# Performance work log

Hardware: AMD Instinct MI355X
Metric: run time of the kernel (lower is better)

The kernel has to match this reference:

```python
import jax, jax.numpy as jnp
import numpy as np

B, M, I = 32, 8192, 256
TEMPERATURE = 1.0


def setup_inputs() -> dict:
    key = jax.random.key(0)
    k1, k2, k3, k4 = jax.random.split(key, 4)
    memory = jax.random.normal(k1, (B, M, I), dtype=jnp.float32)
    qkey = jax.random.normal(k2, (B, I), dtype=jnp.float32)
    beta = jax.random.uniform(k3, (B,), dtype=jnp.float32)
    # xavier-uniform init for Linear(I, I)
    limit = float(np.sqrt(6.0 / (I + I)))
    W = jax.random.uniform(k4, (I, I), dtype=jnp.float32, minval=-limit, maxval=limit)
    b = jnp.zeros((I,), dtype=jnp.float32)
    return {"memory": memory, "key": qkey, "beta": beta, "W": W, "b": b}


def reference(memory, key, beta, W, b):
    # projected_key = tanh(key @ W^T + b)  -- torch Linear stores weight [out, in]
    projected_key = jnp.tanh(key @ W.T + b)                      # [B, I]
    diff = projected_key[:, None, :] - memory                    # [B, M, I]
    distances = jnp.sum(diff * diff, axis=-1)                    # [B, M]
    similarity = -distances
    weights = jax.nn.softmax(beta[:, None] * similarity / TEMPERATURE, axis=-1)  # [B, M]
    read_vector = jnp.einsum('bm,bmi->bi', weights, memory)      # [B, I]
    return weights, read_vector, similarity
```

## Files before the change

### kernel.cpp

```cpp
#include <hip/hip_runtime.h>
#include <math.h>

constexpr int Bdim = 32;
constexpr int Mdim = 8192;
constexpr int Idim = 256;
constexpr int ROWS_PER_BLOCK = 128;
constexpr int ROWS_PER_WAVE = 32;
constexpr int NCHUNK = Mdim / ROWS_PER_BLOCK;

__global__ void proj_key_kernel(const float* __restrict__ key,
                                const float* __restrict__ W,
                                const float* __restrict__ bias,
                                float* __restrict__ pk) {
    int b = blockIdx.x;
    int i = threadIdx.x;
    __shared__ float kq[Idim];
    kq[i] = key[b * Idim + i];
    __syncthreads();
    const float4* w4 = (const float4*)(W + (size_t)i * Idim);
    const float4* k4 = (const float4*)kq;
    float s = bias[i];
    #pragma unroll 4
    for (int k = 0; k < Idim / 4; ++k) {
        float4 wv = w4[k];
        float4 kv = k4[k];
        s += wv.x * kv.x + wv.y * kv.y + wv.z * kv.z + wv.w * kv.w;
    }
    pk[b * Idim + i] = tanhf(s);
}

__global__ void fused_pass1_kernel(const float* __restrict__ memory,
                                   const float* __restrict__ pk,
                                   const float* __restrict__ beta,
                                   float* __restrict__ sim,
                                   float* __restrict__ pvec,
                                   float* __restrict__ pmx,
                                   float* __restrict__ psum) {
    int b = blockIdx.x / NCHUNK;
    int c = blockIdx.x % NCHUNK;
    int wave = threadIdx.x >> 6;
    int lane = threadIdx.x & 63;
    float bt = beta[b];

    float4 pkv = ((const float4*)(pk + b * Idim))[lane];

    int row0 = c * ROWS_PER_BLOCK + wave * ROWS_PER_WAVE;
    const float* base = memory + ((size_t)b * Mdim + row0) * Idim;
    float* simp = sim + (size_t)b * Mdim + row0;

    float mx = -INFINITY, ssum = 0.f;
    float4 acc = make_float4(0.f, 0.f, 0.f, 0.f);
    float my_sim = 0.f;

    for (int r = 0; r < ROWS_PER_WAVE; ++r) {
        float4 mv = ((const float4*)(base + (size_t)r * Idim))[lane];
        float dx = pkv.x - mv.x, dy = pkv.y - mv.y;
        float dz = pkv.z - mv.z, dw = pkv.w - mv.w;
        float s = dx * dx + dy * dy + dz * dz + dw * dw;
        #pragma unroll
        for (int off = 32; off; off >>= 1) s += __shfl_xor(s, off, 64);
        if (lane == r) my_sim = -s;

        float a = -bt * s;
        float nmx = fmaxf(mx, a);
        float scale = __expf(mx - nmx);
        float p = __expf(a - nmx);
        ssum = ssum * scale + p;
        acc.x = acc.x * scale + p * mv.x;
        acc.y = acc.y * scale + p * mv.y;
        acc.z = acc.z * scale + p * mv.z;
        acc.w = acc.w * scale + p * mv.w;
        mx = nmx;
    }
    if (lane < ROWS_PER_WAVE) simp[lane] = my_sim;

    __shared__ float lacc[4][Idim];
    __shared__ float lmx[4], lsum[4];
    ((float4*)lacc[wave])[lane] = acc;
    if (lane == 0) { lmx[wave] = mx; lsum[wave] = ssum; }
    __syncthreads();

    float MX = fmaxf(fmaxf(lmx[0], lmx[1]), fmaxf(lmx[2], lmx[3]));
    float e0 = __expf(lmx[0] - MX), e1 = __expf(lmx[1] - MX);
    float e2 = __expf(lmx[2] - MX), e3 = __expf(lmx[3] - MX);
    int i = threadIdx.x;
    float v = lacc[0][i] * e0 + lacc[1][i] * e1 + lacc[2][i] * e2 + lacc[3][i] * e3;
    size_t pc = (size_t)b * NCHUNK + c;
    pvec[pc * Idim + i] = v;
    if (threadIdx.x == 0) {
        pmx[pc] = MX;
        psum[pc] = lsum[0] * e0 + lsum[1] * e1 + lsum[2] * e2 + lsum[3] * e3;
    }
}

__global__ void combine_kernel(const float* __restrict__ pvec,
                               const float* __restrict__ pmx,
                               const float* __restrict__ psum,
                               float* __restrict__ read_vec,
                               float* __restrict__ MXb,
                               float* __restrict__ invb) {
    int b = blockIdx.x;
    int tid = threadIdx.x;
    __shared__ float e[NCHUNK];
    __shared__ float sInv;

    if (tid < NCHUNK) {
        float m = pmx[(size_t)b * NCHUNK + tid];
        float mm = m;
        #pragma unroll
        for (int off = 32; off; off >>= 1) mm = fmaxf(mm, __shfl_xor(mm, off, 64));
        float ec = __expf(m - mm);
        e[tid] = ec;
        float sc = psum[(size_t)b * NCHUNK + tid] * ec;
        #pragma unroll
        for (int off = 32; off; off >>= 1) sc += __shfl_xor(sc, off, 64);
        if (tid == 0) {
            sInv = 1.f / sc;
            MXb[b] = mm;
            invb[b] = 1.f / sc;
        }
    }
    __syncthreads();

    float v = 0.f;
    const float* p = pvec + (size_t)b * NCHUNK * Idim + tid;
    #pragma unroll 8
    for (int c = 0; c < NCHUNK; ++c) v += p[(size_t)c * Idim] * e[c];
    read_vec[(size_t)b * Idim + tid] = v * sInv;
}

__global__ void weights_kernel(const float* __restrict__ sim,
                               const float* __restrict__ beta,
                               const float* __restrict__ MXb,
                               const float* __restrict__ invb,
                               float* __restrict__ weights) {
    int g = (blockIdx.x * 256 + threadIdx.x) * 4;
    int b = g >> 13;
    float bt = beta[b], MX = MXb[b], inv = invb[b];
    float4 s = *(const float4*)(sim + g);
    float4 w;
    w.x = __expf(bt * s.x - MX) * inv;
    w.y = __expf(bt * s.y - MX) * inv;
    w.z = __expf(bt * s.z - MX) * inv;
    w.w = __expf(bt * s.w - MX) * inv;
    *(float4*)(weights + g) = w;
}

extern "C" void kernel_launch(void* const* d_in, const int* in_sizes, int n_in,
                              void* d_out, int out_size, void* d_ws, size_t ws_size,
                              hipStream_t stream) {
    const float* memory = (const float*)d_in[0];
    const float* key    = (const float*)d_in[1];
    const float* beta   = (const float*)d_in[2];
    const float* W      = (const float*)d_in[3];
    const float* bias   = (const float*)d_in[4];

    float* out = (float*)d_out;
    float* weights  = out;
    float* read_vec = out + (size_t)Bdim * Mdim;
    float* sim      = read_vec + (size_t)Bdim * Idim;

    float* pk   = (float*)d_ws;
    float* pvec = pk + (size_t)Bdim * Idim;
    float* pmx  = pvec + (size_t)Bdim * NCHUNK * Idim;
    float* psum = pmx + (size_t)Bdim * NCHUNK;
    float* MXb  = psum + (size_t)Bdim * NCHUNK;
    float* invb = MXb + Bdim;

    proj_key_kernel<<<Bdim, Idim, 0, stream>>>(key, W, bias, pk);
    fused_pass1_kernel<<<Bdim * NCHUNK, 256, 0, stream>>>(memory, pk, beta,
                                                          sim, pvec, pmx, psum);
    combine_kernel<<<Bdim, Idim, 0, stream>>>(pvec, pmx, psum, read_vec, MXb, invb);
    weights_kernel<<<(Bdim * Mdim) / 1024, 256, 0, stream>>>(sim, beta, MXb, invb, weights);
}
```

Before: 63.94 us.

## Process two rows per wave iteration, lazy rescale, fuse combine with weights kernel

The main pass now splits each wave into two half-waves that each handle one memory row per iteration. Each lane loads two float4s, and the cross-lane reduction drops to 5 shuffles plus one exchange. The online softmax rescales only when a new maximum appears, which removes one exp per row in the common case, and the block reduction now merges 8 partial states. The separate weights kernel is folded into the combine kernel. That saves one launch and the MX/inv round trip, but only 32 blocks are left to write the weights.

```diff
diff --git a/kernel.cpp b/kernel.cpp
--- a/kernel.cpp
+++ b/kernel.cpp
@@ -40,69 +40,104 @@
     int c = blockIdx.x % NCHUNK;
     int wave = threadIdx.x >> 6;
     int lane = threadIdx.x & 63;
+    int half = lane >> 5;
+    int sub  = lane & 31;
     float bt = beta[b];
 
-    float4 pkv = ((const float4*)(pk + b * Idim))[lane];
+    const float4* pk4 = (const float4*)(pk + b * Idim);
+    float4 pk0 = pk4[sub * 2];
+    float4 pk1 = pk4[sub * 2 + 1];
 
     int row0 = c * ROWS_PER_BLOCK + wave * ROWS_PER_WAVE;
     const float* base = memory + ((size_t)b * Mdim + row0) * Idim;
     float* simp = sim + (size_t)b * Mdim + row0;
 
     float mx = -INFINITY, ssum = 0.f;
-    float4 acc = make_float4(0.f, 0.f, 0.f, 0.f);
+    float4 acc0 = make_float4(0.f, 0.f, 0.f, 0.f);
+    float4 acc1 = make_float4(0.f, 0.f, 0.f, 0.f);
     float my_sim = 0.f;
 
-    for (int r = 0; r < ROWS_PER_WAVE; ++r) {
-        float4 mv = ((const float4*)(base + (size_t)r * Idim))[lane];
-        float dx = pkv.x - mv.x, dy = pkv.y - mv.y;
-        float dz = pkv.z - mv.z, dw = pkv.w - mv.w;
-        float s = dx * dx + dy * dy + dz * dz + dw * dw;
-        #pragma unroll
-        for (int off = 32; off; off >>= 1) s += __shfl_xor(s, off, 64);
-        if (lane == r) my_sim = -s;
+    for (int t = 0; t < ROWS_PER_WAVE / 2; ++t) {
+        const float* rp = base + (size_t)(2 * t + half) * Idim + sub * 8;
+        float4 m0 = *(const float4*)rp;
+        float4 m1 = *(const float4*)(rp + 4);
+
+        float d, s;
+        d = pk0.x - m0.x; s  = d * d;
+        d = pk0.y - m0.y; s += d * d;
+        d = pk0.z - m0.z; s += d * d;
+        d = pk0.w - m0.w; s += d * d;
+        d = pk1.x - m1.x; s += d * d;
+        d = pk1.y - m1.y; s += d * d;
+        d = pk1.z - m1.z; s += d * d;
+        d = pk1.w - m1.w; s += d * d;
+        #pragma unroll
+        for (int off = 16; off; off >>= 1) s += __shfl_xor(s, off, 64);
+        float s_other = __shfl_xor(s, 32, 64);
+        if ((lane >> 1) == t) my_sim = (lane & 1) ? -s_other : -s;
 
         float a = -bt * s;
-        float nmx = fmaxf(mx, a);
-        float scale = __expf(mx - nmx);
-        float p = __expf(a - nmx);
-        ssum = ssum * scale + p;
-        acc.x = acc.x * scale + p * mv.x;
-        acc.y = acc.y * scale + p * mv.y;
-        acc.z = acc.z * scale + p * mv.z;
-        acc.w = acc.w * scale + p * mv.w;
-        mx = nmx;
-    }
-    if (lane < ROWS_PER_WAVE) simp[lane] = my_sim;
-
-    __shared__ float lacc[4][Idim];
-    __shared__ float lmx[4], lsum[4];
-    ((float4*)lacc[wave])[lane] = acc;
-    if (lane == 0) { lmx[wave] = mx; lsum[wave] = ssum; }
+        if (a > mx) {
+            float scale = __expf(mx - a);
+            ssum *= scale;
+            acc0.x *= scale; acc0.y *= scale; acc0.z *= scale; acc0.w *= scale;
+            acc1.x *= scale; acc1.y *= scale; acc1.z *= scale; acc1.w *= scale;
+            mx = a;
+        }
+        float p = __expf(a - mx);
+        ssum += p;
+        acc0.x = fmaf(p, m0.x, acc0.x);
+        acc0.y = fmaf(p, m0.y, acc0.y);
+        acc0.z = fmaf(p, m0.z, acc0.z);
+        acc0.w = fmaf(p, m0.w, acc0.w);
+        acc1.x = fmaf(p, m1.x, acc1.x);
+        acc1.y = fmaf(p, m1.y, acc1.y);
+        acc1.z = fmaf(p, m1.z, acc1.z);
+        acc1.w = fmaf(p, m1.w, acc1.w);
+    }
+    if (lane < 32) simp[lane] = my_sim;
+
+    __shared__ float lacc[8][Idim];
+    __shared__ float lmx[8], lsum[8];
+    int wh = wave * 2 + half;
+    ((float4*)(lacc[wh] + sub * 8))[0] = acc0;
+    ((float4*)(lacc[wh] + sub * 8))[1] = acc1;
+    if (sub == 0) { lmx[wh] = mx; lsum[wh] = ssum; }
     __syncthreads();
 
-    float MX = fmaxf(fmaxf(lmx[0], lmx[1]), fmaxf(lmx[2], lmx[3]));
-    float e0 = __expf(lmx[0] - MX), e1 = __expf(lmx[1] - MX);
-    float e2 = __expf(lmx[2] - MX), e3 = __expf(lmx[3] - MX);
+    float MX = lmx[0];
+    #pragma unroll
+    for (int h = 1; h < 8; ++h) MX = fmaxf(MX, lmx[h]);
+    float e[8];
+    #pragma unroll
+    for (int h = 0; h < 8; ++h) e[h] = __expf(lmx[h] - MX);
+
     int i = threadIdx.x;
-    float v = lacc[0][i] * e0 + lacc[1][i] * e1 + lacc[2][i] * e2 + lacc[3][i] * e3;
+    float v = 0.f;
+    #pragma unroll
+    for (int h = 0; h < 8; ++h) v += lacc[h][i] * e[h];
     size_t pc = (size_t)b * NCHUNK + c;
     pvec[pc * Idim + i] = v;
     if (threadIdx.x == 0) {
+        float sc = 0.f;
+        #pragma unroll
+        for (int h = 0; h < 8; ++h) sc += lsum[h] * e[h];
         pmx[pc] = MX;
-        psum[pc] = lsum[0] * e0 + lsum[1] * e1 + lsum[2] * e2 + lsum[3] * e3;
-    }
-}
-
-__global__ void combine_kernel(const float* __restrict__ pvec,
-                               const float* __restrict__ pmx,
-                               const float* __restrict__ psum,
-                               float* __restrict__ read_vec,
-                               float* __restrict__ MXb,
-                               float* __restrict__ invb) {
+        psum[pc] = sc;
+    }
+}
+
+__global__ void combine_weights_kernel(const float* __restrict__ pvec,
+                                       const float* __restrict__ pmx,
+                                       const float* __restrict__ psum,
+                                       const float* __restrict__ sim,
+                                       const float* __restrict__ beta,
+                                       float* __restrict__ read_vec,
+                                       float* __restrict__ weights) {
     int b = blockIdx.x;
     int tid = threadIdx.x;
     __shared__ float e[NCHUNK];
-    __shared__ float sInv;
+    __shared__ float MXs, sInvs;
 
     if (tid < NCHUNK) {
         float m = pmx[(size_t)b * NCHUNK + tid];
@@ -114,36 +149,30 @@
         float sc = psum[(size_t)b * NCHUNK + tid] * ec;
         #pragma unroll
         for (int off = 32; off; off >>= 1) sc += __shfl_xor(sc, off, 64);
-        if (tid == 0) {
-            sInv = 1.f / sc;
-            MXb[b] = mm;
-            invb[b] = 1.f / sc;
-        }
+        if (tid == 0) { MXs = mm; sInvs = 1.f / sc; }
     }
     __syncthreads();
+
+    float MX = MXs, inv = sInvs;
 
     float v = 0.f;
     const float* p = pvec + (size_t)b * NCHUNK * Idim + tid;
     #pragma unroll 8
     for (int c = 0; c < NCHUNK; ++c) v += p[(size_t)c * Idim] * e[c];
-    read_vec[(size_t)b * Idim + tid] = v * sInv;
-}
-
-__global__ void weights_kernel(const float* __restrict__ sim,
-                               const float* __restrict__ beta,
-                               const float* __restrict__ MXb,
-                               const float* __restrict__ invb,
-                               float* __restrict__ weights) {
-    int g = (blockIdx.x * 256 + threadIdx.x) * 4;
-    int b = g >> 13;
-    float bt = beta[b], MX = MXb[b], inv = invb[b];
-    float4 s = *(const float4*)(sim + g);
-    float4 w;
-    w.x = __expf(bt * s.x - MX) * inv;
-    w.y = __expf(bt * s.y - MX) * inv;
-    w.z = __expf(bt * s.z - MX) * inv;
-    w.w = __expf(bt * s.w - MX) * inv;
-    *(float4*)(weights + g) = w;
+    read_vec[(size_t)b * Idim + tid] = v * inv;
+
+    float bt = beta[b];
+    const float4* s4 = (const float4*)(sim + (size_t)b * Mdim);
+    float4* w4 = (float4*)(weights + (size_t)b * Mdim);
+    for (int m4 = tid; m4 < Mdim / 4; m4 += 256) {
+        float4 s = s4[m4];
+        float4 w;
+        w.x = __expf(bt * s.x - MX) * inv;
+        w.y = __expf(bt * s.y - MX) * inv;
+        w.z = __expf(bt * s.z - MX) * inv;
+        w.w = __expf(bt * s.w - MX) * inv;
+        w4[m4] = w;
+    }
 }
 
 extern "C" void kernel_launch(void* const* d_in, const int* in_sizes, int n_in,
@@ -164,12 +193,10 @@
     float* pvec = pk + (size_t)Bdim * Idim;
     float* pmx  = pvec + (size_t)Bdim * NCHUNK * Idim;
     float* psum = pmx + (size_t)Bdim * NCHUNK;
-    float* MXb  = psum + (size_t)Bdim * NCHUNK;
-    float* invb = MXb + Bdim;
 
     proj_key_kernel<<<Bdim, Idim, 0, stream>>>(key, W, bias, pk);
     fused_pass1_kernel<<<Bdim * NCHUNK, 256, 0, stream>>>(memory, pk, beta,
                                                           sim, pvec, pmx, psum);
-    combine_kernel<<<Bdim, Idim, 0, stream>>>(pvec, pmx, psum, read_vec, MXb, invb);
-    weights_kernel<<<(Bdim * Mdim) / 1024, 256, 0, stream>>>(sim, beta, MXb, invb, weights);
-}
+    combine_weights_kernel<<<Bdim, 256, 0, stream>>>(pvec, pmx, psum, sim, beta,
+                                                     read_vec, weights);
+}
```

Result: slower. 65.37 us (+2.2%).

## Prefetch rows in pass1, lazy rescale, and fuse combine with weights kernel

Applied to the files above, without the earlier changes.

The main pass loop now software-prefetches memory rows two ahead. The online softmax rescales only when a new maximum appears, using FMAs, which saves an exp per row in the common case. The combine and weights kernels are merged into one epilogue launch of Bdim*NSLICE blocks. Each block recomputes the per-batch max and normalizer, and slice 0 also produces the read vector. This removes one kernel launch and the intermediate MXb/invb buffers, at the cost of redundant per-slice reductions and a divergent branch in the inner loop.

```diff
diff --git a/kernel.cpp b/kernel.cpp
--- a/kernel.cpp
+++ b/kernel.cpp
@@ -7,6 +7,7 @@
 constexpr int ROWS_PER_BLOCK = 128;
 constexpr int ROWS_PER_WAVE = 32;
 constexpr int NCHUNK = Mdim / ROWS_PER_BLOCK;
+constexpr int NSLICE = 8;
 
 __global__ void proj_key_kernel(const float* __restrict__ key,
                                 const float* __restrict__ W,
@@ -52,27 +53,42 @@
     float4 acc = make_float4(0.f, 0.f, 0.f, 0.f);
     float my_sim = 0.f;
 
-    for (int r = 0; r < ROWS_PER_WAVE; ++r) {
-        float4 mv = ((const float4*)(base + (size_t)r * Idim))[lane];
+    auto body = [&](float4 mv, int r) {
         float dx = pkv.x - mv.x, dy = pkv.y - mv.y;
         float dz = pkv.z - mv.z, dw = pkv.w - mv.w;
         float s = dx * dx + dy * dy + dz * dz + dw * dw;
         #pragma unroll
         for (int off = 32; off; off >>= 1) s += __shfl_xor(s, off, 64);
         if (lane == r) my_sim = -s;
+        float a = -bt * s;
+        if (a > mx) {
+            float sc = __expf(mx - a);
+            ssum *= sc;
+            acc.x *= sc; acc.y *= sc; acc.z *= sc; acc.w *= sc;
+            mx = a;
+        }
+        float p = __expf(a - mx);
+        ssum += p;
+        acc.x = fmaf(p, mv.x, acc.x);
+        acc.y = fmaf(p, mv.y, acc.y);
+        acc.z = fmaf(p, mv.z, acc.z);
+        acc.w = fmaf(p, mv.w, acc.w);
+    };
 
-        float a = -bt * s;
-        float nmx = fmaxf(mx, a);
-        float scale = __expf(mx - nmx);
-        float p = __expf(a - nmx);
-        ssum = ssum * scale + p;
-        acc.x = acc.x * scale + p * mv.x;
-        acc.y = acc.y * scale + p * mv.y;
-        acc.z = acc.z * scale + p * mv.z;
-        acc.w = acc.w * scale + p * mv.w;
-        mx = nmx;
+    const float4* rp = (const float4*)base + lane;
+    float4 cur = rp[0];
+    float4 nxt = rp[64];
+    #pragma unroll 2
+    for (int r = 0; r < ROWS_PER_WAVE - 2; ++r) {
+        float4 pf = rp[(size_t)(r + 2) * 64];
+        body(cur, r);
+        cur = nxt;
+        nxt = pf;
     }
-    if (lane < ROWS_PER_WAVE) simp[lane] = my_sim;
+    body(cur, ROWS_PER_WAVE - 2);
+    body(nxt, ROWS_PER_WAVE - 1);
+
+    if (lane < 32) simp[lane] = my_sim;
 
     __shared__ float lacc[4][Idim];
     __shared__ float lmx[4], lsum[4];
@@ -93,16 +109,18 @@
     }
 }
 
-__global__ void combine_kernel(const float* __restrict__ pvec,
-                               const float* __restrict__ pmx,
-                               const float* __restrict__ psum,
-                               float* __restrict__ read_vec,
-                               float* __restrict__ MXb,
-                               float* __restrict__ invb) {
-    int b = blockIdx.x;
+__global__ void epilogue_kernel(const float* __restrict__ pvec,
+                                const float* __restrict__ pmx,
+                                const float* __restrict__ psum,
+                                const float* __restrict__ sim,
+                                const float* __restrict__ beta,
+                                float* __restrict__ read_vec,
+                                float* __restrict__ weights) {
+    int b = blockIdx.x / NSLICE;
+    int slice = blockIdx.x % NSLICE;
     int tid = threadIdx.x;
     __shared__ float e[NCHUNK];
-    __shared__ float sInv;
+    __shared__ float MXs, sInvs;
 
     if (tid < NCHUNK) {
         float m = pmx[(size_t)b * NCHUNK + tid];
@@ -114,36 +132,29 @@
         float sc = psum[(size_t)b * NCHUNK + tid] * ec;
         #pragma unroll
         for (int off = 32; off; off >>= 1) sc += __shfl_xor(sc, off, 64);
-        if (tid == 0) {
-            sInv = 1.f / sc;
-            MXb[b] = mm;
-            invb[b] = 1.f / sc;
-        }
+        if (tid == 0) { MXs = mm; sInvs = 1.f / sc; }
     }
     __syncthreads();
 
-    float v = 0.f;
-    const float* p = pvec + (size_t)b * NCHUNK * Idim + tid;
-    #pragma unroll 8
-    for (int c = 0; c < NCHUNK; ++c) v += p[(size_t)c * Idim] * e[c];
-    read_vec[(size_t)b * Idim + tid] = v * sInv;
-}
+    float MX = MXs, inv = sInvs;
 
-__global__ void weights_kernel(const float* __restrict__ sim,
-                               const float* __restrict__ beta,
-                               const float* __restrict__ MXb,
-                               const float* __restrict__ invb,
-                               float* __restrict__ weights) {
-    int g = (blockIdx.x * 256 + threadIdx.x) * 4;
-    int b = g >> 13;
-    float bt = beta[b], MX = MXb[b], inv = invb[b];
-    float4 s = *(const float4*)(sim + g);
+    if (slice == 0) {
+        float v = 0.f;
+        const float* p = pvec + (size_t)b * NCHUNK * Idim + tid;
+        #pragma unroll 8
+        for (int c = 0; c < NCHUNK; ++c) v += p[(size_t)c * Idim] * e[c];
+        read_vec[(size_t)b * Idim + tid] = v * inv;
+    }
+
+    float bt = beta[b];
+    int m4 = slice * (Mdim / NSLICE / 4) + tid;
+    float4 s = ((const float4*)(sim + (size_t)b * Mdim))[m4];
     float4 w;
     w.x = __expf(bt * s.x - MX) * inv;
     w.y = __expf(bt * s.y - MX) * inv;
     w.z = __expf(bt * s.z - MX) * inv;
     w.w = __expf(bt * s.w - MX) * inv;
-    *(float4*)(weights + g) = w;
+    ((float4*)(weights + (size_t)b * Mdim))[m4] = w;
 }
 
 extern "C" void kernel_launch(void* const* d_in, const int* in_sizes, int n_in,
@@ -164,12 +175,10 @@
     float* pvec = pk + (size_t)Bdim * Idim;
     float* pmx  = pvec + (size_t)Bdim * NCHUNK * Idim;
     float* psum = pmx + (size_t)Bdim * NCHUNK;
-    float* MXb  = psum + (size_t)Bdim * NCHUNK;
-    float* invb = MXb + Bdim;
 
     proj_key_kernel<<<Bdim, Idim, 0, stream>>>(key, W, bias, pk);
     fused_pass1_kernel<<<Bdim * NCHUNK, 256, 0, stream>>>(memory, pk, beta,
                                                           sim, pvec, pmx, psum);
-    combine_kernel<<<Bdim, Idim, 0, stream>>>(pvec, pmx, psum, read_vec, MXb, invb);
-    weights_kernel<<<(Bdim * Mdim) / 1024, 256, 0, stream>>>(sim, beta, MXb, invb, weights);
+    epilogue_kernel<<<Bdim * NSLICE, 256, 0, stream>>>(pvec, pmx, psum, sim, beta,
+                                                       read_vec, weights);
 }
```

Measured after the change: 62.35 us. 1.03x faster.
